# Kernel optimization log

Hardware: AMD Instinct MI355X
Metric: run time of the kernel (lower is better)

Reference implementation:

```python
import jax, jax.numpy as jnp
import numpy as np

N, E = 10000, 160000
IN, C, H = 64, 256, 8


def gat_layer(x, src, dst, W, a_src, a_dst, b, heads, ch, n, concat=True):
    # linear transform per head: [n, heads, ch]
    h = (x @ W).reshape(n, heads, ch)
    al_s = jnp.sum(h * a_src, axis=-1)  # [n, heads]
    al_d = jnp.sum(h * a_dst, axis=-1)  # [n, heads]
    e = jax.nn.leaky_relu(al_s[src] + al_d[dst], 0.2)  # [E, heads]
    # segment softmax over incoming edges of each dst node
    m = jax.ops.segment_max(e, dst, num_segments=n)
    m = jnp.where(jnp.isfinite(m), m, 0.0)  # guard empty segments
    p = jnp.exp(e - m[dst])
    s = jax.ops.segment_sum(p, dst, num_segments=n)
    alpha = p / (s[dst] + 1e-16)  # [E, heads]
    # scatter-aggregate weighted source features
    out = jax.ops.segment_sum(h[src] * alpha[:, :, None], dst, num_segments=n)
    out = out.reshape(n, heads * ch) if concat else out.mean(axis=1)
    return jax.nn.elu(out + b)


def setup_inputs() -> dict:
    key = jax.random.key(0)
    ks = jax.random.split(key, 16)
    sc = 0.05
    x = jax.random.normal(ks[0], (N, IN), dtype=jnp.float32)
    edge_index = jax.random.randint(ks[1], (2, E), 0, N)
    W1 = jax.random.normal(ks[2], (IN, H * C), dtype=jnp.float32) * sc
    as1 = jax.random.normal(ks[3], (H, C), dtype=jnp.float32) * sc
    ad1 = jax.random.normal(ks[4], (H, C), dtype=jnp.float32) * sc
    b1 = jnp.zeros((H * C,), dtype=jnp.float32)
    W2 = jax.random.normal(ks[5], (H * C, H * C), dtype=jnp.float32) * sc
    as2 = jax.random.normal(ks[6], (H, C), dtype=jnp.float32) * sc
    ad2 = jax.random.normal(ks[7], (H, C), dtype=jnp.float32) * sc
    b2 = jnp.zeros((H * C,), dtype=jnp.float32)
    W3 = jax.random.normal(ks[8], (H * C, C), dtype=jnp.float32) * sc
    as3 = jax.random.normal(ks[9], (1, C), dtype=jnp.float32) * sc
    ad3 = jax.random.normal(ks[10], (1, C), dtype=jnp.float32) * sc
    b3 = jnp.zeros((C,), dtype=jnp.float32)
    return {"x": x, "edge_index": edge_index,
            "W1": W1, "as1": as1, "ad1": ad1, "b1": b1,
            "W2": W2, "as2": as2, "ad2": ad2, "b2": b2,
            "W3": W3, "as3": as3, "ad3": ad3, "b3": b3}


def reference(x, edge_index, W1, as1, ad1, b1, W2, as2, ad2, b2, W3, as3, ad3, b3):
    src, dst = edge_index[0], edge_index[1]
    h = gat_layer(x, src, dst, W1, as1, ad1, b1, H, C, N, concat=True)
    h = gat_layer(h, src, dst, W2, as2, ad2, b2, H, C, N, concat=True)
    h = gat_layer(h, src, dst, W3, as3, ad3, b3, 1, C, N, concat=True)
    return h
```

## Files before the change

### kernel.cpp

```cpp
#include <hip/hip_runtime.h>


typedef __attribute__((ext_vector_type(8))) short bf16x8;
typedef __attribute__((ext_vector_type(4))) float f32x4;

#define DEVINL __device__ __forceinline__

static constexpr int NN   = 10000;
static constexpr int NE   = 160000;
static constexpr int MPAD = 10240;
static constexpr int DIN  = 64;
static constexpr int CCH  = 256;
static constexpr int NH   = 8;
static constexpr int F12  = 2048;
static constexpr int PSTR = MPAD*NH;

DEVINL unsigned short f2bf(float x){
  unsigned u = __float_as_uint(x);
  u += 0x7fffu + ((u >> 16) & 1u);
  return (unsigned short)(u >> 16);
}
DEVINL float bf2f(unsigned short h){ return __uint_as_float(((unsigned)h) << 16); }

DEVINL void gload_lds16(const unsigned short* g, unsigned short* lds){
  __builtin_amdgcn_global_load_lds(
      (__attribute__((address_space(1))) unsigned int*)(g),
      (__attribute__((address_space(3))) unsigned int*)(lds), 16, 0, 0);
}

__global__ __launch_bounds__(256) void transpose_cvt_kernel(const float* __restrict__ W,
                                                            unsigned short* __restrict__ Wt,
                                                            int K, int Nn){
  __shared__ float tile[32][33];
  int k0 = blockIdx.x*32, n0 = blockIdx.y*32;
  int tx = threadIdx.x & 31, ty = threadIdx.x >> 5;
  #pragma unroll
  for (int r = ty; r < 32; r += 8) tile[r][tx] = W[(size_t)(k0+r)*Nn + n0 + tx];
  __syncthreads();
  #pragma unroll
  for (int r = ty; r < 32; r += 8) Wt[(size_t)(n0+r)*K + k0 + tx] = f2bf(tile[tx][r]);
}

__global__ __launch_bounds__(256) void hist_kernel(const int* __restrict__ dst,
                                                   int* __restrict__ deg, int E_){
  int i = blockIdx.x*256 + threadIdx.x;
  if (i < E_) atomicAdd(&deg[dst[i]], 1);
}

__global__ __launch_bounds__(256) void scan_kernel(const int* __restrict__ deg,
                                                   int* __restrict__ off, int n){
  const int CH = (n + 255) / 256;
  int t = threadIdx.x;
  int lo = t*CH, hi = min(lo + CH, n);
  int s = 0;
  for (int i = lo; i < hi; i++) s += deg[i];
  __shared__ int ws[256];
  ws[t] = s;
  __syncthreads();
  for (int d = 1; d < 256; d <<= 1){
    int v = (t >= d) ? ws[t-d] : 0;
    __syncthreads();
    ws[t] += v;
    __syncthreads();
  }
  int run = ws[t] - s;
  for (int i = lo; i < hi; i++){ off[i] = run; run += deg[i]; }
  if (t == 255) off[n] = ws[255];
}

__global__ __launch_bounds__(256) void scatter_kernel(const int* __restrict__ src,
                                                      const int* __restrict__ dst,
                                                      const int* __restrict__ off,
                                                      int* __restrict__ cursor,
                                                      int* __restrict__ csrc, int E_){
  int i = blockIdx.x*256 + threadIdx.x;
  if (i >= E_) return;
  int d = dst[i];
  int pI = atomicAdd(&cursor[d], 1);
  csrc[off[d] + pI] = src[i];
}

__global__ __launch_bounds__(256) void wa1_kernel(const float* __restrict__ W1,
                                                  const float* __restrict__ a1s,
                                                  const float* __restrict__ a1d,
                                                  float* __restrict__ Wa1){
  int t = blockIdx.x*256 + threadIdx.x;
  if (t >= 64*16) return;
  int c = t >> 4, i = t & 15;
  int h = i & 7;
  const float* a = (i < 8) ? a1s : a1d;
  float s = 0.f;
  #pragma unroll 8
  for (int j = 0; j < 256; j++) s = fmaf(W1[(size_t)c*F12 + h*256 + j], a[h*256 + j], s);
  Wa1[c*16 + i] = s;
}

__global__ __launch_bounds__(256) void logits1_kernel(const float* __restrict__ x,
                                                      const float* __restrict__ Wa1,
                                                      float* __restrict__ als,
                                                      float* __restrict__ ald){
  __shared__ float wa[64*16];
  for (int i = threadIdx.x; i < 64*16; i += 256) wa[i] = Wa1[i];
  __syncthreads();
  int gid = blockIdx.x*256 + threadIdx.x;
  int v = gid >> 4, i = gid & 15;
  if (v >= NN) return;
  float s = 0.f;
  #pragma unroll
  for (int c = 0; c < 64; c++) s = fmaf(x[(size_t)v*64 + c], wa[c*16 + i], s);
  if (i < 8) als[v*8 + i] = s;
  else       ald[v*8 + (i - 8)] = s;
}

__global__ __launch_bounds__(256) void combine_kernel(const float* __restrict__ pls,
                                                      const float* __restrict__ pld,
                                                      float* __restrict__ als,
                                                      float* __restrict__ ald,
                                                      int count){
  int i = blockIdx.x*256 + threadIdx.x;
  if (i >= count) return;
  als[i] = (pls[i] + pls[PSTR + i]) + (pls[2*PSTR + i] + pls[3*PSTR + i]);
  ald[i] = (pld[i] + pld[PSTR + i]) + (pld[2*PSTR + i] + pld[3*PSTR + i]);
}

__global__ __launch_bounds__(256) void agg1_kernel(const float* __restrict__ x,
                                                   const int* __restrict__ off,
                                                   const int* __restrict__ csrc,
                                                   const float* __restrict__ als,
                                                   const float* __restrict__ ald,
                                                   unsigned short* __restrict__ Xa){
  const int wv = threadIdx.x >> 6, lane = threadIdx.x & 63;
  const int v = blockIdx.x*4 + wv;
  if (v >= NN) return;
  const int e0 = off[v], deg = off[v+1] - e0;
  const int h  = lane & 7;
  const int es = lane >> 3;

  __shared__ float al_sh[4][64];
  __shared__ int   u_sh[4][8];

  const float aldv = ald[v*8 + h];

  float m = -1e30f, s = 0.f;
  for (int i = es; i < deg; i += 8){
    int u = csrc[e0 + i];
    float xe = als[u*8 + h] + aldv;
    xe = xe > 0.f ? xe : 0.2f*xe;
    float nm = fmaxf(m, xe);
    s = s*__expf(m - nm) + __expf(xe - nm);
    m = nm;
  }
  #pragma unroll
  for (int d = 8; d < 64; d <<= 1){
    float mo = __shfl_xor(m, d);
    float so = __shfl_xor(s, d);
    float nm = fmaxf(m, mo);
    s = s*__expf(m - nm) + so*__expf(mo - nm);
    m = nm;
  }
  const float sinv = 1.f / (s + 1e-16f);

  float acc[8];
  #pragma unroll
  for (int hh = 0; hh < 8; hh++) acc[hh] = 0.f;

  const int nfull = deg & ~7;
  for (int base = 0; base < nfull; base += 8){
    int u = csrc[e0 + base + es];
    if (h == 0) u_sh[wv][es] = u;
    float xe = als[u*8 + h] + aldv;
    xe = xe > 0.f ? xe : 0.2f*xe;
    al_sh[wv][es*8 + h] = __expf(xe - m) * sinv;
    #pragma unroll
    for (int j = 0; j < 8; j++){
      float xv = x[(size_t)u_sh[wv][j]*64 + lane];
      #pragma unroll
      for (int hh = 0; hh < 8; hh++)
        acc[hh] = fmaf(al_sh[wv][j*8 + hh], xv, acc[hh]);
    }
  }
  if (nfull < deg){
    const int nch = deg - nfull;
    if (es < nch){
      int u = csrc[e0 + nfull + es];
      if (h == 0) u_sh[wv][es] = u;
      float xe = als[u*8 + h] + aldv;
      xe = xe > 0.f ? xe : 0.2f*xe;
      al_sh[wv][es*8 + h] = __expf(xe - m) * sinv;
    }
    for (int j = 0; j < nch; j++){
      float xv = x[(size_t)u_sh[wv][j]*64 + lane];
      #pragma unroll
      for (int hh = 0; hh < 8; hh++)
        acc[hh] = fmaf(al_sh[wv][j*8 + hh], xv, acc[hh]);
    }
  }

  #pragma unroll
  for (int hh = 0; hh < 8; hh++)
    Xa[(size_t)v*512 + hh*64 + lane] = f2bf(acc[hh]);
}

__global__ __launch_bounds__(256) void gemm_l1_kernel(
    const unsigned short* __restrict__ Xa,
    const unsigned short* __restrict__ Wt1,
    const float* __restrict__ b1,
    unsigned short* __restrict__ actA)
{
  __shared__ __align__(16) unsigned short As[2][128*32];
  __shared__ __align__(16) unsigned short Bs[2][256*32];
  const int wave = threadIdx.x >> 6, lane = threadIdx.x & 63;
  const int wm = wave >> 1, wn = wave & 1;
  const size_t m0 = (size_t)blockIdx.x * 128;
  const int h = blockIdx.y;
  const int lr = lane >> 2, l3 = lane & 3;

  #pragma unroll
  for (int sB = 0; sB < 2; sB++){
    #pragma unroll
    for (int j = 0; j < 2; j++){
      int rb = (wave*2 + j)*16;
      int row = rb + lr;
      int kc = l3 ^ ((row >> 1) & 3);
      gload_lds16(Xa + (m0 + row)*512 + h*64 + sB*32 + kc*8, &As[sB][rb*32]);
    }
    #pragma unroll
    for (int j = 0; j < 4; j++){
      int rb = (wave*4 + j)*16;
      int row = rb + lr;
      int kc = l3 ^ ((row >> 1) & 3);
      gload_lds16(Wt1 + (size_t)(h*256 + row)*64 + sB*32 + kc*8, &Bs[sB][rb*32]);
    }
  }
  asm volatile("s_waitcnt vmcnt(0)" ::: "memory");
  __syncthreads();

  f32x4 acc[4][8];
  #pragma unroll
  for (int i = 0; i < 4; i++)
    #pragma unroll
    for (int j = 0; j < 8; j++) acc[i][j] = (f32x4){0.f,0.f,0.f,0.f};

  const int rl = lane & 15, q = lane >> 4;
  #pragma unroll
  for (int sB = 0; sB < 2; sB++){
    bf16x8 af[4], bfr[8];
    #pragma unroll
    for (int mm = 0; mm < 4; mm++){
      int row = wm*64 + mm*16 + rl;
      int ch = q ^ ((row >> 1) & 3);
      af[mm] = *(const bf16x8*)&As[sB][row*32 + ch*8];
    }
    #pragma unroll
    for (int n = 0; n < 8; n++){
      int row = wn*128 + n*16 + rl;
      int ch = q ^ ((row >> 1) & 3);
      bfr[n] = *(const bf16x8*)&Bs[sB][row*32 + ch*8];
    }
    #pragma unroll
    for (int mm = 0; mm < 4; mm++)
      #pragma unroll
      for (int n = 0; n < 8; n++)
        acc[mm][n] = __builtin_amdgcn_mfma_f32_16x16x32_bf16(af[mm], bfr[n], acc[mm][n], 0, 0, 0);
  }

  #pragma unroll
  for (int mm = 0; mm < 4; mm++)
    #pragma unroll
    for (int n = 0; n < 8; n++)
      #pragma unroll
      for (int r = 0; r < 4; r++){
        size_t row = m0 + wm*64 + mm*16 + q*4 + r;
        int col = wn*128 + n*16 + rl;
        float o = acc[mm][n][r] + b1[h*256 + col];
        o = o > 0.f ? o : (__expf(o) - 1.f);
        actA[row*F12 + h*256 + col] = f2bf(o);
      }
}

__global__ __launch_bounds__(512, 1) void gemm_l2_kernel(
    const unsigned short* __restrict__ A,
    const unsigned short* __restrict__ Bt,
    unsigned short* __restrict__ Chm,
    const float* __restrict__ as2,
    const float* __restrict__ ad2,
    float* __restrict__ pls,
    float* __restrict__ pld,
    int K)
{
  __shared__ __align__(16) unsigned short As[3][640*32];
  __shared__ __align__(16) unsigned short Bs[3][128*32];

  const int tid  = threadIdx.x;
  const int wave = tid >> 6, lane = tid & 63;
  const int wm = wave >> 1, wn = wave & 1;

  const int orig = blockIdx.x;
  const int wg   = (orig & 7) * 32 + (orig >> 3);
  const size_t m0 = (size_t)(wg >> 4) * 640;
  const size_t n0 = (size_t)(wg & 15) * 128;

  f32x4 acc[10][4];
  #pragma unroll
  for (int i = 0; i < 10; i++)
    #pragma unroll
    for (int j = 0; j < 4; j++) acc[i][j] = (f32x4){0.f,0.f,0.f,0.f};

  const int lr = lane >> 2;
  const int l3 = lane & 3;

  auto stageA = [&](int slot, int k0, int j){
    const int rb  = (wave*5 + j) * 16;
    const int row = rb + lr;
    const int kc  = l3 ^ ((row >> 1) & 3);
    gload_lds16(A + (m0 + row)*(size_t)K + k0 + kc*8, &As[slot][rb*32]);
  };
  auto stageB = [&](int slot, int k0){
    const int rb  = wave * 16;
    const int row = rb + lr;
    const int kc  = l3 ^ ((row >> 1) & 3);
    gload_lds16(Bt + (n0 + row)*(size_t)K + k0 + kc*8, &Bs[slot][rb*32]);
  };
  auto stageTile = [&](int T){
    const int slot = T % 3, k0 = T << 5;
    #pragma unroll
    for (int j = 0; j < 5; j++) stageA(slot, k0, j);
    stageB(slot, k0);
  };

  const int nt = K >> 5;
  stageTile(0);
  stageTile(1);

  const int rl = lane & 15;
  const int q  = lane >> 4;

  for (int T = 0; T < nt; ++T){
    if (T + 1 < nt) asm volatile("s_waitcnt vmcnt(6)" ::: "memory");
    else            asm volatile("s_waitcnt vmcnt(0)" ::: "memory");
    __builtin_amdgcn_s_barrier();

    const int slot = T % 3;
    const bool st  = (T + 2 < nt);
    const int s2   = (T + 2) % 3;
    const int k2   = (T + 2) << 5;

    bf16x8 bfr[4], af[5];
    #pragma unroll
    for (int n = 0; n < 4; n++){
      const int row = wn*64 + n*16 + rl;
      const int ch  = q ^ ((row >> 1) & 3);
      bfr[n] = *(const bf16x8*)&Bs[slot][row*32 + ch*8];
    }
    #pragma unroll
    for (int m = 0; m < 5; m++){
      const int row = wm*160 + m*16 + rl;
      const int ch  = q ^ ((row >> 1) & 3);
      af[m] = *(const bf16x8*)&As[slot][row*32 + ch*8];
    }
    if (st){ stageA(s2, k2, 0); stageA(s2, k2, 1); stageA(s2, k2, 2); }
    asm volatile("s_waitcnt lgkmcnt(0)" ::: "memory");
    __builtin_amdgcn_sched_barrier(0);
    __builtin_amdgcn_s_setprio(1);
    #pragma unroll
    for (int m = 0; m < 5; m++)
      #pragma unroll
      for (int n = 0; n < 4; n++)
        acc[m][n] = __builtin_amdgcn_mfma_f32_16x16x32_bf16(af[m], bfr[n], acc[m][n], 0, 0, 0);
    __builtin_amdgcn_s_setprio(0);
    __builtin_amdgcn_sched_barrier(0);
    #pragma unroll
    for (int m = 0; m < 5; m++){
      const int row = wm*160 + (m+5)*16 + rl;
      const int ch  = q ^ ((row >> 1) & 3);
      af[m] = *(const bf16x8*)&As[slot][row*32 + ch*8];
    }
    if (st){ stageA(s2, k2, 3); stageA(s2, k2, 4); stageB(s2, k2); }
    asm volatile("s_waitcnt lgkmcnt(0)" ::: "memory");
    __builtin_amdgcn_sched_barrier(0);
    __builtin_amdgcn_s_setprio(1);
    #pragma unroll
    for (int m = 0; m < 5; m++)
      #pragma unroll
      for (int n = 0; n < 4; n++)
        acc[m+5][n] = __builtin_amdgcn_mfma_f32_16x16x32_bf16(af[m], bfr[n], acc[m+5][n], 0, 0, 0);
    __builtin_amdgcn_s_setprio(0);
  }

  const int head = (int)(n0 >> 8);
  const int pslot = (((int)(n0 >> 7) & 1) << 1) | wn;
  float asw[4], adw[4];
  #pragma unroll
  for (int n = 0; n < 4; n++){
    const int ch = (int)(n0 & 255) + wn*64 + n*16 + rl;
    asw[n] = as2[head*CCH + ch];
    adw[n] = ad2[head*CCH + ch];
  }
  #pragma unroll
  for (int m = 0; m < 10; m++)
    #pragma unroll
    for (int r = 0; r < 4; r++){
      const size_t row = m0 + wm*160 + m*16 + q*4 + r;
      float ps = 0.f, pd = 0.f;
      #pragma unroll
      for (int n = 0; n < 4; n++){
        const float cv = acc[m][n][r];
        ps = fmaf(cv, asw[n], ps);
        pd = fmaf(cv, adw[n], pd);
        const int ch = wn*64 + n*16 + rl + (int)(n0 & 255);
        Chm[((size_t)head*MPAD + row)*CCH + ch] = f2bf(cv);
      }
      #pragma unroll
      for (int d = 1; d < 16; d <<= 1){
        ps += __shfl_xor(ps, d);
        pd += __shfl_xor(pd, d);
      }
      if (rl == 0){
        pls[(size_t)pslot*PSTR + row*NH + head] = ps;
        pld[(size_t)pslot*PSTR + row*NH + head] = pd;
      }
    }
}

__global__ __launch_bounds__(256, 2) void gemm_bt_kernel(
    const unsigned short* __restrict__ A,
    const unsigned short* __restrict__ Bt,
    unsigned short* __restrict__ C,
    const float* __restrict__ as3,
    const float* __restrict__ ad3,
    float* __restrict__ pls,
    float* __restrict__ pld,
    int K, int Nn)
{
  __shared__ __align__(16) unsigned short As[2][128*32];
  __shared__ __align__(16) unsigned short Bs[2][128*32];
  const int tid  = threadIdx.x;
  const int wave = tid >> 6, lane = tid & 63;
  const int wr = wave >> 1, wc = wave & 1;
  const size_t m0 = (size_t)blockIdx.x * 128;
  const size_t n0 = (size_t)blockIdx.y * 128;

  const int l4 = lane >> 2;
  const int lc = lane & 3;

  f32x4 acc[4][4];
  #pragma unroll
  for (int i = 0; i < 4; i++)
    #pragma unroll
    for (int j = 0; j < 4; j++) acc[i][j] = (f32x4){0.f,0.f,0.f,0.f};

  auto stage = [&](int buf, int kt){
    const int k0 = kt << 5;
    #pragma unroll
    for (int half = 0; half < 2; ++half){
      const int rb  = (wave + half*4) * 16;
      const int row = rb + l4;
      const int kc  = lc ^ ((row >> 1) & 3);
      gload_lds16(A + ((m0 + row)*(size_t)K + k0 + kc*8), &As[buf][rb*32]);
    }
    #pragma unroll
    for (int half = 0; half < 2; ++half){
      const int rb  = (wave + half*4) * 16;
      const int row = rb + l4;
      const int kc  = lc ^ ((row >> 1) & 3);
      gload_lds16(Bt + ((n0 + row)*(size_t)K + k0 + kc*8), &Bs[buf][rb*32]);
    }
  };

  const int nt = K >> 5;
  stage(0, 0);
  __syncthreads();

  const int rl = lane & 15;
  const int q  = lane >> 4;

  int cur = 0;
  for (int t = 0; t < nt; ++t){
    if (t + 1 < nt) stage(cur ^ 1, t + 1);
    bf16x8 af[4], bfr[4];
    #pragma unroll
    for (int m = 0; m < 4; m++){
      int row = wr*64 + m*16 + rl;
      int ch  = q ^ ((row >> 1) & 3);
      af[m] = *(const bf16x8*)&As[cur][row*32 + ch*8];
    }
    #pragma unroll
    for (int n = 0; n < 4; n++){
      int row = wc*64 + n*16 + rl;
      int ch  = q ^ ((row >> 1) & 3);
      bfr[n] = *(const bf16x8*)&Bs[cur][row*32 + ch*8];
    }
    #pragma unroll
    for (int m = 0; m < 4; m++)
      #pragma unroll
      for (int n = 0; n < 4; n++)
        acc[m][n] = __builtin_amdgcn_mfma_f32_16x16x32_bf16(af[m], bfr[n], acc[m][n], 0, 0, 0);
    __syncthreads();
    cur ^= 1;
  }

  float asw[4], adw[4];
  #pragma unroll
  for (int n = 0; n < 4; n++){
    const int ch = (int)n0 + wc*64 + n*16 + rl;
    asw[n] = as3[ch];
    adw[n] = ad3[ch];
  }
  const int pslot = (((int)(n0 >> 7)) << 1) | wc;
  #pragma unroll
  for (int m = 0; m < 4; m++)
    #pragma unroll
    for (int r = 0; r < 4; r++){
      const size_t row = m0 + wr*64 + m*16 + q*4 + r;
      float ps = 0.f, pd = 0.f;
      #pragma unroll
      for (int n = 0; n < 4; n++){
        const float cv = acc[m][n][r];
        ps = fmaf(cv, asw[n], ps);
        pd = fmaf(cv, adw[n], pd);
        const size_t col = n0 + wc*64 + n*16 + rl;
        C[row*(size_t)Nn + col] = f2bf(cv);
      }
      #pragma unroll
      for (int d = 1; d < 16; d <<= 1){
        ps += __shfl_xor(ps, d);
        pd += __shfl_xor(pd, d);
      }
      if (rl == 0){
        pls[(size_t)pslot*PSTR + row] = ps;
        pld[(size_t)pslot*PSTR + row] = pd;
      }
    }
}

template<int NHD>
__global__ __launch_bounds__(256) void aggw_kernel(
    const unsigned short* __restrict__ Hm,
    const int* __restrict__ off, const int* __restrict__ csrc,
    const float* __restrict__ als, const float* __restrict__ ald,
    const float* __restrict__ bias,
    unsigned short* __restrict__ actout,
    float* __restrict__ fout)
{
  const int wv = threadIdx.x >> 6, lane = threadIdx.x & 63;
  const int hl = lane >> 5;
  const int li = lane & 31;
  int v, h;
  if constexpr (NHD == 8){
    h = blockIdx.x & 7;
    v = (blockIdx.x >> 3) * 4 + wv;
  } else {
    h = 0;
    v = blockIdx.x * 4 + wv;
  }
  if (v >= NN) return;
  const int e0 = off[v], deg = off[v+1] - e0;
  const float aldv = ald[v*NHD + h];

  __shared__ float al_sh[4][64];
  __shared__ int   u_sh[4][64];

  float mloc = -1e30f;
  for (int i = lane; i < deg; i += 64){
    int u = csrc[e0 + i];
    float xe = als[u*NHD + h] + aldv;
    xe = xe > 0.f ? xe : 0.2f*xe;
    mloc = fmaxf(mloc, xe);
  }
  #pragma unroll
  for (int d = 1; d < 64; d <<= 1) mloc = fmaxf(mloc, __shfl_xor(mloc, d));
  float sloc = 0.f;
  for (int i = lane; i < deg; i += 64){
    int u = csrc[e0 + i];
    float xe = als[u*NHD + h] + aldv;
    xe = xe > 0.f ? xe : 0.2f*xe;
    sloc += __expf(xe - mloc);
  }
  #pragma unroll
  for (int d = 1; d < 64; d <<= 1) sloc += __shfl_xor(sloc, d);
  const float sinv = 1.f / (sloc + 1e-16f);

  const unsigned short* hB = Hm + (size_t)h*MPAD*CCH + li*8;
  float acc[8];
  #pragma unroll
  for (int k = 0; k < 8; k++) acc[k] = 0.f;

  auto edge_fma = [&](const uint4& w, float a){
    acc[0] = fmaf(a, bf2f((unsigned short)(w.x & 0xffff)), acc[0]);
    acc[1] = fmaf(a, bf2f((unsigned short)(w.x >> 16)),    acc[1]);
    acc[2] = fmaf(a, bf2f((unsigned short)(w.y & 0xffff)), acc[2]);
    acc[3] = fmaf(a, bf2f((unsigned short)(w.y >> 16)),    acc[3]);
    acc[4] = fmaf(a, bf2f((unsigned short)(w.z & 0xffff)), acc[4]);
    acc[5] = fmaf(a, bf2f((unsigned short)(w.z >> 16)),    acc[5]);
    acc[6] = fmaf(a, bf2f((unsigned short)(w.w & 0xffff)), acc[6]);
    acc[7] = fmaf(a, bf2f((unsigned short)(w.w >> 16)),    acc[7]);
  };

  for (int base = 0; base < deg; base += 64){
    const int nch = min(deg - base, 64);
    if (lane < nch){
      int u = csrc[e0 + base + lane];
      u_sh[wv][lane] = u;
      float xe = als[u*NHD + h] + aldv;
      xe = xe > 0.f ? xe : 0.2f*xe;
      al_sh[wv][lane] = __expf(xe - mloc) * sinv;
    }
    int j = 0;
    for (; j + 4 <= nch; j += 4){
      const int   ua = u_sh[wv][j + hl],     ub = u_sh[wv][j + 2 + hl];
      const float aa = al_sh[wv][j + hl],    ab = al_sh[wv][j + 2 + hl];
      uint4 wA = *(const uint4*)(hB + (size_t)ua*CCH);
      uint4 wB = *(const uint4*)(hB + (size_t)ub*CCH);
      edge_fma(wA, aa);
      edge_fma(wB, ab);
    }
    for (; j + 2 <= nch; j += 2){
      const int   ua = u_sh[wv][j + hl];
      const float aa = al_sh[wv][j + hl];
      uint4 wA = *(const uint4*)(hB + (size_t)ua*CCH);
      edge_fma(wA, aa);
    }
    if (j < nch && hl == 0){
      const int   ua = u_sh[wv][j];
      const float aa = al_sh[wv][j];
      uint4 wA = *(const uint4*)(hB + (size_t)ua*CCH);
      edge_fma(wA, aa);
    }
  }

  #pragma unroll
  for (int k = 0; k < 8; k++) acc[k] += __shfl_xor(acc[k], 32);

  if (hl == 0){
    const int c0 = h*CCH + li*8;
    float o[8];
    #pragma unroll
    for (int k = 0; k < 8; k++){
      o[k] = acc[k] + bias[c0 + k];
      o[k] = o[k] > 0.f ? o[k] : (__expf(o[k]) - 1.f);
    }
    if constexpr (NHD == 8){
      bf16x8 ov;
      #pragma unroll
      for (int k = 0; k < 8; k++) ov[k] = (short)f2bf(o[k]);
      *(bf16x8*)&actout[(size_t)v*F12 + c0] = ov;
    } else {
      float4 o0 = make_float4(o[0], o[1], o[2], o[3]);
      float4 o1 = make_float4(o[4], o[5], o[6], o[7]);
      *(float4*)(fout + (size_t)v*CCH + li*8)     = o0;
      *(float4*)(fout + (size_t)v*CCH + li*8 + 4) = o1;
    }
  }
}

extern "C" void kernel_launch(void* const* d_in, const int* in_sizes, int n_in,
                              void* d_out, int out_size, void* d_ws, size_t ws_size,
                              hipStream_t stream)
{
  const float* x   = (const float*)d_in[0];
  const int*   ei  = (const int*)d_in[1];
  const float* W1  = (const float*)d_in[2];
  const float* as1 = (const float*)d_in[3];
  const float* ad1 = (const float*)d_in[4];
  const float* b1  = (const float*)d_in[5];
  const float* W2  = (const float*)d_in[6];
  const float* as2 = (const float*)d_in[7];
  const float* ad2 = (const float*)d_in[8];
  const float* b2  = (const float*)d_in[9];
  const float* W3  = (const float*)d_in[10];
  const float* as3 = (const float*)d_in[11];
  const float* ad3 = (const float*)d_in[12];
  const float* b3  = (const float*)d_in[13];
  float* out = (float*)d_out;
  (void)in_sizes; (void)n_in; (void)out_size; (void)ws_size;

  char* p = (char*)d_ws;
  auto carve = [&](size_t bytes)->char* {
    char* r = p; p += (bytes + 255) & ~(size_t)255; return r;
  };
  unsigned short* actA = (unsigned short*)carve((size_t)MPAD*F12*2);
  unsigned short* hbuf = (unsigned short*)carve((size_t)MPAD*F12*2);
  unsigned short* Wt1  = (unsigned short*)carve((size_t)F12*DIN*2);
  unsigned short* Wt2  = (unsigned short*)carve((size_t)F12*F12*2);
  unsigned short* Wt3  = (unsigned short*)carve((size_t)CCH*F12*2);
  float* als  = (float*)carve((size_t)NN*NH*4);
  float* ald  = (float*)carve((size_t)NN*NH*4);
  float* pls  = (float*)carve((size_t)4*PSTR*4);
  float* pld  = (float*)carve((size_t)4*PSTR*4);
  float* Wa1  = (float*)carve((size_t)64*16*4);
  int* deg    = (int*)carve((size_t)2*NN*4);
  int* cursor = deg + NN;
  int* off    = (int*)carve((size_t)(NN+1)*4);
  int* csrc   = (int*)carve((size_t)NE*4);
  unsigned short* Xa = hbuf;

  const int* esrc = ei;
  const int* edst = ei + NE;

  transpose_cvt_kernel<<<dim3(DIN/32,  F12/32), 256, 0, stream>>>(W1, Wt1, DIN, F12);
  transpose_cvt_kernel<<<dim3(F12/32,  F12/32), 256, 0, stream>>>(W2, Wt2, F12, F12);
  transpose_cvt_kernel<<<dim3(F12/32,  CCH/32), 256, 0, stream>>>(W3, Wt3, F12, CCH);

  hipMemsetAsync(deg, 0, (size_t)2*NN*4, stream);
  hist_kernel<<<(NE + 255)/256, 256, 0, stream>>>(edst, deg, NE);
  scan_kernel<<<1, 256, 0, stream>>>(deg, off, NN);
  scatter_kernel<<<(NE + 255)/256, 256, 0, stream>>>(esrc, edst, off, cursor, csrc, NE);

  wa1_kernel<<<4, 256, 0, stream>>>(W1, as1, ad1, Wa1);
  logits1_kernel<<<(NN*16 + 255)/256, 256, 0, stream>>>(x, Wa1, als, ald);
  hipMemsetAsync(Xa + (size_t)NN*512, 0, (size_t)(MPAD-NN)*512*2, stream);
  agg1_kernel<<<(NN + 3)/4, 256, 0, stream>>>(x, off, csrc, als, ald, Xa);
  gemm_l1_kernel<<<dim3(MPAD/128, NH), 256, 0, stream>>>(Xa, Wt1, b1, actA);

  gemm_l2_kernel<<<256, 512, 0, stream>>>(actA, Wt2, hbuf, as2, ad2, pls, pld, F12);
  combine_kernel<<<(NN*NH + 255)/256, 256, 0, stream>>>(pls, pld, als, ald, NN*NH);
  aggw_kernel<8><<<((NN + 3)/4)*8, 256, 0, stream>>>(hbuf, off, csrc, als, ald, b2, actA, nullptr);

  gemm_bt_kernel<<<dim3(MPAD/128, CCH/128), 256, 0, stream>>>(actA, Wt3, hbuf, as3, ad3, pls, pld, F12, CCH);
  combine_kernel<<<(NN + 255)/256, 256, 0, stream>>>(pls, pld, als, ald, NN);
  aggw_kernel<1><<<(NN + 3)/4, 256, 0, stream>>>(hbuf, off, csrc, als, ald, b3, nullptr, out);
}
```

Before: 322.6 us.

## Restructure layer-3 GEMM with 160-row tiles, 128-block grid, and explicit prefetch pipeline

The layer-3 GEMM now uses 160x128 tiles so that a grid of exactly 128 blocks covers the padded rows, with a remapped block index. Loads are split by wave: waves 0-1 fetch A and waves 2-3 fetch B. The loop is now a two-stage prefetch ring synchronised with explicit vmcnt/lgkmcnt waits and raw barriers, and s_setprio is raised around the MFMA section. The goal is to fill the CUs in a single wave and to overlap global-to-LDS loads with MFMA work. The trade-off is more accumulator registers and fragile hand-written wait counts.

```diff
diff --git a/kernel.cpp b/kernel.cpp
--- a/kernel.cpp
+++ b/kernel.cpp
@@ -422,7 +422,7 @@
     }
 }
 
-__global__ __launch_bounds__(256, 2) void gemm_bt_kernel(
+__global__ __launch_bounds__(256, 2) void gemm_l3_kernel(
     const unsigned short* __restrict__ A,
     const unsigned short* __restrict__ Bt,
     unsigned short* __restrict__ C,
@@ -430,96 +430,118 @@
     const float* __restrict__ ad3,
     float* __restrict__ pls,
     float* __restrict__ pld,
-    int K, int Nn)
+    int K)
 {
-  __shared__ __align__(16) unsigned short As[2][128*32];
+  __shared__ __align__(16) unsigned short As[2][160*32];
   __shared__ __align__(16) unsigned short Bs[2][128*32];
+
   const int tid  = threadIdx.x;
   const int wave = tid >> 6, lane = tid & 63;
-  const int wr = wave >> 1, wc = wave & 1;
-  const size_t m0 = (size_t)blockIdx.x * 128;
-  const size_t n0 = (size_t)blockIdx.y * 128;
-
-  const int l4 = lane >> 2;
-  const int lc = lane & 3;
-
-  f32x4 acc[4][4];
-  #pragma unroll
-  for (int i = 0; i < 4; i++)
+  const int wm = wave >> 1, wn = wave & 1;
+
+  const int orig = blockIdx.x;
+  const int wg   = (orig & 7) * 16 + (orig >> 3);
+  const int nb   = wg & 1;
+  const size_t m0 = (size_t)(wg >> 1) * 160;
+  const size_t n0 = (size_t)nb * 128;
+
+  f32x4 acc[5][4];
+  #pragma unroll
+  for (int i = 0; i < 5; i++)
     #pragma unroll
     for (int j = 0; j < 4; j++) acc[i][j] = (f32x4){0.f,0.f,0.f,0.f};
 
-  auto stage = [&](int buf, int kt){
-    const int k0 = kt << 5;
-    #pragma unroll
-    for (int half = 0; half < 2; ++half){
-      const int rb  = (wave + half*4) * 16;
-      const int row = rb + l4;
-      const int kc  = lc ^ ((row >> 1) & 3);
-      gload_lds16(A + ((m0 + row)*(size_t)K + k0 + kc*8), &As[buf][rb*32]);
-    }
-    #pragma unroll
-    for (int half = 0; half < 2; ++half){
-      const int rb  = (wave + half*4) * 16;
-      const int row = rb + l4;
-      const int kc  = lc ^ ((row >> 1) & 3);
-      gload_lds16(Bt + ((n0 + row)*(size_t)K + k0 + kc*8), &Bs[buf][rb*32]);
+  const int lr = lane >> 2;
+  const int l3 = lane & 3;
+
+  const int nIss = (wave < 2) ? 5 : 4;
+  auto stageT = [&](int T){
+    const int slot = T & 1, k0 = T << 5;
+    if (wave < 2){
+      #pragma unroll
+      for (int j = 0; j < 5; j++){
+        const int rb  = (wave*5 + j) * 16;
+        const int row = rb + lr;
+        const int kc  = l3 ^ ((row >> 1) & 3);
+        gload_lds16(A + (m0 + row)*(size_t)K + k0 + kc*8, &As[slot][rb*32]);
+      }
+    } else {
+      #pragma unroll
+      for (int j = 0; j < 4; j++){
+        const int rb  = ((wave - 2)*4 + j) * 16;
+        const int row = rb + lr;
+        const int kc  = l3 ^ ((row >> 1) & 3);
+        gload_lds16(Bt + (n0 + row)*(size_t)K + k0 + kc*8, &Bs[slot][rb*32]);
+      }
     }
   };
 
   const int nt = K >> 5;
-  stage(0, 0);
-  __syncthreads();
+  stageT(0);
+  stageT(1);
 
   const int rl = lane & 15;
   const int q  = lane >> 4;
 
-  int cur = 0;
-  for (int t = 0; t < nt; ++t){
-    if (t + 1 < nt) stage(cur ^ 1, t + 1);
-    bf16x8 af[4], bfr[4];
-    #pragma unroll
-    for (int m = 0; m < 4; m++){
-      int row = wr*64 + m*16 + rl;
-      int ch  = q ^ ((row >> 1) & 3);
+  for (int T = 0; T < nt; ++T){
+    if (T + 1 < nt){
+      if (wave < 2) asm volatile("s_waitcnt vmcnt(5)" ::: "memory");
+      else          asm volatile("s_waitcnt vmcnt(4)" ::: "memory");
+    } else {
+      asm volatile("s_waitcnt vmcnt(0)" ::: "memory");
+    }
+    __builtin_amdgcn_s_barrier();
+
+    const int cur = T & 1;
+    bf16x8 af[5], bfr[4];
+    #pragma unroll
+    for (int m = 0; m < 5; m++){
+      const int row = wm*80 + m*16 + rl;
+      const int ch  = q ^ ((row >> 1) & 3);
       af[m] = *(const bf16x8*)&As[cur][row*32 + ch*8];
     }
     #pragma unroll
     for (int n = 0; n < 4; n++){
-      int row = wc*64 + n*16 + rl;
-      int ch  = q ^ ((row >> 1) & 3);
+      const int row = wn*64 + n*16 + rl;
+      const int ch  = q ^ ((row >> 1) & 3);
       bfr[n] = *(const bf16x8*)&Bs[cur][row*32 + ch*8];
     }
-    #pragma unroll
-    for (int m = 0; m < 4; m++)
+    asm volatile("s_waitcnt lgkmcnt(0)" ::: "memory");
+    __builtin_amdgcn_sched_barrier(0);
+    __builtin_amdgcn_s_barrier();
+
+    if (T + 2 < nt) stageT(T + 2);
+
+    __builtin_amdgcn_s_setprio(1);
+    #pragma unroll
+    for (int m = 0; m < 5; m++)
       #pragma unroll
       for (int n = 0; n < 4; n++)
         acc[m][n] = __builtin_amdgcn_mfma_f32_16x16x32_bf16(af[m], bfr[n], acc[m][n], 0, 0, 0);
-    __syncthreads();
-    cur ^= 1;
+    __builtin_amdgcn_s_setprio(0);
   }
 
   float asw[4], adw[4];
   #pragma unroll
   for (int n = 0; n < 4; n++){
-    const int ch = (int)n0 + wc*64 + n*16 + rl;
+    const int ch = (int)n0 + wn*64 + n*16 + rl;
     asw[n] = as3[ch];
     adw[n] = ad3[ch];
   }
-  const int pslot = (((int)(n0 >> 7)) << 1) | wc;
-  #pragma unroll
-  for (int m = 0; m < 4; m++)
+  const int pslot = (nb << 1) | wn;
+  #pragma unroll
+  for (int m = 0; m < 5; m++)
     #pragma unroll
     for (int r = 0; r < 4; r++){
-      const size_t row = m0 + wr*64 + m*16 + q*4 + r;
+      const size_t row = m0 + wm*80 + m*16 + q*4 + r;
       float ps = 0.f, pd = 0.f;
       #pragma unroll
       for (int n = 0; n < 4; n++){
         const float cv = acc[m][n][r];
         ps = fmaf(cv, asw[n], ps);
         pd = fmaf(cv, adw[n], pd);
-        const size_t col = n0 + wc*64 + n*16 + rl;
-        C[row*(size_t)Nn + col] = f2bf(cv);
+        const size_t col = n0 + wn*64 + n*16 + rl;
+        C[row*(size_t)CCH + col] = f2bf(cv);
       }
       #pragma unroll
       for (int d = 1; d < 16; d <<= 1){
@@ -716,7 +738,7 @@
   combine_kernel<<<(NN*NH + 255)/256, 256, 0, stream>>>(pls, pld, als, ald, NN*NH);
   aggw_kernel<8><<<((NN + 3)/4)*8, 256, 0, stream>>>(hbuf, off, csrc, als, ald, b2, actA, nullptr);
 
-  gemm_bt_kernel<<<dim3(MPAD/128, CCH/128), 256, 0, stream>>>(actA, Wt3, hbuf, as3, ad3, pls, pld, F12, CCH);
+  gemm_l3_kernel<<<128, 256, 0, stream>>>(actA, Wt3, hbuf, as3, ad3, pls, pld, F12);
   combine_kernel<<<(NN + 255)/256, 256, 0, stream>>>(pls, pld, als, ald, NN);
   aggw_kernel<1><<<(NN + 3)/4, 256, 0, stream>>>(hbuf, off, csrc, als, ald, b3, nullptr, out);
 }
```

Measured after the change: 314.9 us. -2.4%, faster.
